# Kernel tuning notes

Measured on AMD Instinct MI355X. Metric: run time of the kernel, lower is better.

## Reference

```python
import jax, jax.numpy as jnp
import numpy as np

DIN = 1024   # input_embedding_size
D = 128      # embedding_size
N, T = 4, 4096


def setup_inputs() -> dict:
    key = jax.random.key(0)
    kx, kq, kk, kv = jax.random.split(key, 4)
    x = jax.random.normal(kx, (N, T, DIN), dtype=jnp.float32)
    # torch Linear(DIN, D, bias=False): weight [D, DIN], y = x @ W.T.
    # Store transposed [DIN, D] so q = x @ Wq is the same math.
    s = 1.0 / np.sqrt(DIN)
    Wq = jax.random.uniform(kq, (DIN, D), jnp.float32, -s, s)
    Wk = jax.random.uniform(kk, (DIN, D), jnp.float32, -s, s)
    Wv = jax.random.uniform(kv, (DIN, D), jnp.float32, -s, s)
    return {"x": x, "Wq": Wq, "Wk": Wk, "Wv": Wv}


def reference(x, Wq, Wk, Wv):
    # x: [N,T,DIN]
    q = jnp.einsum('ntc,cd->ntd', x, Wq)  # [N,T,D]
    k = jnp.einsum('ntc,cd->ntd', x, Wk)
    v = jnp.einsum('ntc,cd->ntd', x, Wv)
    att = jnp.einsum('ntd,nsd->nts', q, k)  # [N,T,T], no 1/sqrt(D) scaling (faithful)
    Tlen = x.shape[1]
    causal = jnp.tril(jnp.ones((Tlen, Tlen), dtype=bool))
    # faithful to torch: tril() zeros upper triangle, then masked_fill(att == 0, -inf)
    att = jnp.where(causal, att, 0.0)
    att = jnp.where(att == 0.0, -jnp.inf, att)
    att = jax.nn.softmax(att, axis=-1)  # [N,T,T]
    out = jnp.einsum('nts,nsd->ntd', att, v)  # [N,T,D]
    return out, att
```

## Files before the change

### kernel.cpp

```cpp
#include <hip/hip_runtime.h>

typedef _Float16 f16;
typedef __attribute__((ext_vector_type(8))) _Float16 f16x8;
typedef __attribute__((ext_vector_type(8))) short s16x8;
typedef __attribute__((ext_vector_type(4))) float f32x4;
typedef __attribute__((ext_vector_type(4))) unsigned short us16x4;

#define DIN   1024
#define DD    128
#define NBAT  4
#define TLEN  4096
#define NROWS (NBAT * TLEN)

static __device__ __forceinline__ unsigned short f2bf(float f) {
  unsigned int u = __builtin_bit_cast(unsigned int, f);
  u = (u + 0x7fffu + ((u >> 16) & 1u)) >> 16;
  return (unsigned short)u;
}
static __device__ __forceinline__ float bf2f(unsigned short h) {
  return __builtin_bit_cast(float, (unsigned int)h << 16);
}
static __device__ __forceinline__ unsigned short f2h(float f) {
  _Float16 h = (_Float16)f;
  return __builtin_bit_cast(unsigned short, h);
}

static __device__ __forceinline__ int swz128(int d, int key) {
  return ((((d >> 3) ^ key) & 15) << 3) | (d & 7);
}
static __device__ __forceinline__ int swz64(int c, int key) {
  return ((((c >> 3) ^ key) & 7) << 3) | (c & 7);
}

typedef __attribute__((address_space(1))) const unsigned int* gas1_t;
typedef __attribute__((address_space(3))) unsigned int* las3_t;
static __device__ __forceinline__ void gload16(const void* g, void* l) {
  __builtin_amdgcn_global_load_lds((gas1_t)g, (las3_t)l, 16, 0, 0);
}

__global__ void build_wt(const float* __restrict__ Wq, const float* __restrict__ Wk,
                         const float* __restrict__ Wv,
                         unsigned short* __restrict__ Wh, unsigned short* __restrict__ Wl) {
  int col = blockIdx.x;
  const float* W = (col < 128) ? Wq : (col < 256 ? Wk : Wv);
  int j = col & 127;
  for (int kk = (int)threadIdx.x; kk < DIN; kk += blockDim.x) {
    float w = W[(size_t)kk * DD + j];
    unsigned short h = f2bf(w);
    unsigned short l = f2bf(w - bf2f(h));
    int c64 = kk >> 6, w64 = kk & 63;
    int kks = (c64 << 6) + swz64(w64, col & 7);
    Wh[(size_t)col * DIN + kks] = h;
    Wl[(size_t)col * DIN + kks] = l;
  }
}

__global__ __launch_bounds__(256, 2) void proj_qkv(
    const float* __restrict__ x,
    const unsigned short* __restrict__ Wh, const unsigned short* __restrict__ Wl,
    unsigned short* __restrict__ qws, unsigned short* __restrict__ kws,
    unsigned short* __restrict__ vws) {
  __shared__ __align__(16) unsigned short Ah[128 * 64];
  __shared__ __align__(16) unsigned short Al[128 * 64];
  __shared__ __align__(16) unsigned short Bh[128 * 64];
  __shared__ __align__(16) unsigned short Bl[128 * 64];

  const int tid = (int)threadIdx.x;
  const int lane = tid & 63;
  const int wid = tid >> 6;
  const int t0 = blockIdx.x * 128;
  const int ct = blockIdx.y;

  const int rbase = (wid >> 1) * 64;
  const int cbase = (wid & 1) * 64;

  f32x4 acc[4][4];
#pragma unroll
  for (int m = 0; m < 4; ++m)
#pragma unroll
    for (int n = 0; n < 4; ++n) acc[m][n] = f32x4{0.f, 0.f, 0.f, 0.f};

  for (int kr = 0; kr < 16; ++kr) {
#pragma unroll
    for (int rr = 0; rr < 8; ++rr) {
      int idx = rr * 256 + tid;
      int row = idx >> 4;
      int c0 = (idx & 15) * 4;
      f32x4 xv = *(const f32x4*)(x + (size_t)(t0 + row) * DIN + kr * 64 + c0);
      int g = swz64(c0, row & 7);
      unsigned short hs0 = f2bf(xv[0]), hs1 = f2bf(xv[1]), hs2 = f2bf(xv[2]), hs3 = f2bf(xv[3]);
      us16x4 hv = {hs0, hs1, hs2, hs3};
      us16x4 lv = {f2bf(xv[0] - bf2f(hs0)), f2bf(xv[1] - bf2f(hs1)),
                   f2bf(xv[2] - bf2f(hs2)), f2bf(xv[3] - bf2f(hs3))};
      *(us16x4*)&Ah[row * 64 + g] = hv;
      *(us16x4*)&Al[row * 64 + g] = lv;
    }
#pragma unroll
    for (int rr = 0; rr < 4; ++rr) {
      int idx = rr * 256 + tid;
      int row = idx >> 3;
      int g = idx & 7;
      size_t gbyte = ((size_t)(ct * 128 + row) * DIN + (size_t)kr * 64) * 2 + (size_t)g * 16;
      gload16((const char*)Wh + gbyte, (char*)Bh + (size_t)idx * 16);
      gload16((const char*)Wl + gbyte, (char*)Bl + (size_t)idx * 16);
    }
    __syncthreads();

#pragma unroll
    for (int kc = 0; kc < 2; ++kc) {
      s16x8 ah[4], al[4], bh[4], bl[4];
#pragma unroll
      for (int m = 0; m < 4; ++m) {
        int r = rbase + m * 16 + (lane & 15);
        int g = ((kc * 4 + (lane >> 4)) ^ (r & 7)) * 8;
        ah[m] = *(const s16x8*)&Ah[r * 64 + g];
        al[m] = *(const s16x8*)&Al[r * 64 + g];
      }
#pragma unroll
      for (int n = 0; n < 4; ++n) {
        int c = cbase + n * 16 + (lane & 15);
        int g = ((kc * 4 + (lane >> 4)) ^ (c & 7)) * 8;
        bh[n] = *(const s16x8*)&Bh[c * 64 + g];
        bl[n] = *(const s16x8*)&Bl[c * 64 + g];
      }
#pragma unroll
      for (int m = 0; m < 4; ++m)
#pragma unroll
        for (int n = 0; n < 4; ++n) {
          acc[m][n] = __builtin_amdgcn_mfma_f32_16x16x32_bf16(ah[m], bh[n], acc[m][n], 0, 0, 0);
          acc[m][n] = __builtin_amdgcn_mfma_f32_16x16x32_bf16(ah[m], bl[n], acc[m][n], 0, 0, 0);
          acc[m][n] = __builtin_amdgcn_mfma_f32_16x16x32_bf16(al[m], bh[n], acc[m][n], 0, 0, 0);
        }
    }
    __syncthreads();
  }

#pragma unroll
  for (int m = 0; m < 4; ++m)
#pragma unroll
    for (int n = 0; n < 4; ++n)
#pragma unroll
      for (int e = 0; e < 4; ++e) {
        int t = t0 + rbase + m * 16 + (lane >> 4) * 4 + e;
        int d = cbase + n * 16 + (lane & 15);
        unsigned short hv = f2h(acc[m][n][e]);
        if (ct == 0) {
          qws[(size_t)t * DD + swz128(d, t & 7)] = hv;
        } else if (ct == 1) {
          kws[(size_t)t * DD + swz128(d, t & 7)] = hv;
        } else {
          int nb = t >> 12, tl = t & (TLEN - 1);
          int ch = tl >> 7, wpos = tl & 127;
          int tls = ch * 128 + swz128(wpos, d & 7);
          vws[((size_t)nb * DD + d) * TLEN + tls] = hv;
        }
      }
}

__global__ __launch_bounds__(256, 2) void attn_fused(
    const unsigned short* __restrict__ qws, const unsigned short* __restrict__ kws,
    const unsigned short* __restrict__ vws, float* __restrict__ out,
    float* __restrict__ att) {
  __shared__ __align__(16) unsigned short kl[128 * 128];
  __shared__ __align__(16) unsigned short vl[128 * 128];
  __shared__ __align__(16) unsigned short qp[64 * 128];

  const int tid = (int)threadIdx.x;
  const int lane = tid & 63;
  const int wid = tid >> 6;
  const int qi = blockIdx.x;
  const int n = blockIdx.y;
  const int t0 = qi * 64;

  {
    const char* gq = (const char*)(qws + (size_t)(n * TLEN + t0) * DD);
#pragma unroll
    for (int rr = 0; rr < 4; ++rr) {
      int idx = rr * 256 + tid;
      gload16(gq + (size_t)idx * 16, (char*)qp + (size_t)idx * 16);
    }
  }
  __syncthreads();
  f16x8 qa[4];
  {
    int r = wid * 16 + (lane & 15);
#pragma unroll
    for (int kc = 0; kc < 4; ++kc) {
      int g = ((kc * 4 + (lane >> 4)) ^ (r & 7)) * 8;
      qa[kc] = *(const f16x8*)&qp[r * 128 + g];
    }
  }
  __syncthreads();

  const int jmax = (t0 + 63) >> 7;
  const int rowg0 = t0 + wid * 16 + (lane >> 4) * 4;

  float zacc[4] = {0.f, 0.f, 0.f, 0.f};
  for (int j = 0; j <= jmax; ++j) {
    const char* gk = (const char*)(kws + (size_t)(n * TLEN + j * 128) * DD);
#pragma unroll
    for (int rr = 0; rr < 8; ++rr) {
      int idx = rr * 256 + tid;
      gload16(gk + (size_t)idx * 16, (char*)kl + (size_t)idx * 16);
    }
    __syncthreads();
#pragma unroll
    for (int fc = 0; fc < 8; ++fc) {
      f32x4 s = f32x4{0.f, 0.f, 0.f, 0.f};
      int rc = fc * 16 + (lane & 15);
#pragma unroll
      for (int kc = 0; kc < 4; ++kc) {
        int g = ((kc * 4 + (lane >> 4)) ^ (rc & 7)) * 8;
        f16x8 kb = *(const f16x8*)&kl[rc * 128 + g];
        s = __builtin_amdgcn_mfma_f32_16x16x32_f16(qa[kc], kb, s, 0, 0, 0);
      }
      int colg = j * 128 + rc;
#pragma unroll
      for (int e = 0; e < 4; ++e) {
        float sv = s[e];
        int rowg = rowg0 + e;
        float ev = (colg <= rowg && sv != 0.0f) ? __expf(sv) : 0.0f;
        zacc[e] += ev;
      }
    }
    __syncthreads();
  }
  float rz[4];
#pragma unroll
  for (int e = 0; e < 4; ++e) {
    float z = zacc[e];
    z += __shfl_xor(z, 1);
    z += __shfl_xor(z, 2);
    z += __shfl_xor(z, 4);
    z += __shfl_xor(z, 8);
    rz[e] = (z > 0.f) ? (1.0f / z) : 0.0f;
  }

  f32x4 oacc[8];
#pragma unroll
  for (int fd = 0; fd < 8; ++fd) oacc[fd] = f32x4{0.f, 0.f, 0.f, 0.f};
  float* attn_base = att + (size_t)n * TLEN * TLEN;

  for (int j = 0; j <= jmax; ++j) {
    const char* gk = (const char*)(kws + (size_t)(n * TLEN + j * 128) * DD);
#pragma unroll
    for (int rr = 0; rr < 8; ++rr) {
      int idx = rr * 256 + tid;
      gload16(gk + (size_t)idx * 16, (char*)kl + (size_t)idx * 16);
    }
    {
      const char* gv = (const char*)(vws + (size_t)n * DD * TLEN);
#pragma unroll
      for (int rr = 0; rr < 8; ++rr) {
        int idx = rr * 256 + tid;
        int d = idx >> 4;
        size_t gb = ((size_t)d * TLEN + (size_t)j * 128) * 2 + (size_t)(idx & 15) * 16;
        gload16(gv + gb, (char*)vl + (size_t)idx * 16);
      }
    }
    __syncthreads();

#pragma unroll
    for (int fc = 0; fc < 8; ++fc) {
      f32x4 s = f32x4{0.f, 0.f, 0.f, 0.f};
      int cloc = fc * 16 + (lane & 15);
#pragma unroll
      for (int kc = 0; kc < 4; ++kc) {
        int g = ((kc * 4 + (lane >> 4)) ^ (cloc & 7)) * 8;
        f16x8 kb = *(const f16x8*)&kl[cloc * 128 + g];
        s = __builtin_amdgcn_mfma_f32_16x16x32_f16(qa[kc], kb, s, 0, 0, 0);
      }
      int colg = j * 128 + cloc;
#pragma unroll
      for (int e = 0; e < 4; ++e) {
        float sv = s[e];
        int rowg = rowg0 + e;
        float ev = (colg <= rowg && sv != 0.0f) ? __expf(sv) : 0.0f;
        float p = ev * rz[e];
        int rq = wid * 16 + (lane >> 4) * 4 + e;
        qp[rq * 128 + swz128(cloc, rq & 7)] = f2h(p);
        attn_base[(size_t)rowg * TLEN + colg] = p;
      }
    }
    __syncthreads();

#pragma unroll
    for (int kc = 0; kc < 4; ++kc) {
      int rp = wid * 16 + (lane & 15);
      int gp = ((kc * 4 + (lane >> 4)) ^ (rp & 7)) * 8;
      f16x8 pa = *(const f16x8*)&qp[rp * 128 + gp];
#pragma unroll
      for (int fd = 0; fd < 8; ++fd) {
        int dv = fd * 16 + (lane & 15);
        int gvv = ((kc * 4 + (lane >> 4)) ^ (dv & 7)) * 8;
        f16x8 vb = *(const f16x8*)&vl[dv * 128 + gvv];
        oacc[fd] = __builtin_amdgcn_mfma_f32_16x16x32_f16(pa, vb, oacc[fd], 0, 0, 0);
      }
    }
    __syncthreads();
  }

#pragma unroll
  for (int fd = 0; fd < 8; ++fd)
#pragma unroll
    for (int e = 0; e < 4; ++e) {
      int t = t0 + wid * 16 + (lane >> 4) * 4 + e;
      int d = fd * 16 + (lane & 15);
      out[(size_t)(n * TLEN + t) * DD + d] = oacc[fd][e];
    }

  int c0 = (jmax + 1) * 128;
  f32x4 z4 = f32x4{0.f, 0.f, 0.f, 0.f};
  for (int r = 0; r < 64; ++r) {
    float* rowp = attn_base + (size_t)(t0 + r) * TLEN;
    for (int c = c0 + tid * 4; c < TLEN; c += 1024) {
      *(f32x4*)(rowp + c) = z4;
    }
  }
}

extern "C" void kernel_launch(void* const* d_in, const int* in_sizes, int n_in,
                              void* d_out, int out_size, void* d_ws, size_t ws_size,
                              hipStream_t stream) {
  const float* x  = (const float*)d_in[0];
  const float* Wq = (const float*)d_in[1];
  const float* Wk = (const float*)d_in[2];
  const float* Wv = (const float*)d_in[3];

  float* out = (float*)d_out;
  float* att = out + (size_t)NBAT * TLEN * DD;

  unsigned short* ws = (unsigned short*)d_ws;
  unsigned short* Wh  = ws;
  unsigned short* Wl  = Wh + (size_t)384 * DIN;
  unsigned short* qws = Wl + (size_t)384 * DIN;
  unsigned short* kws = qws + (size_t)NROWS * DD;
  unsigned short* vws = kws + (size_t)NROWS * DD;

  build_wt<<<dim3(384), dim3(256), 0, stream>>>(Wq, Wk, Wv, Wh, Wl);
  proj_qkv<<<dim3(128, 3), dim3(256), 0, stream>>>(x, Wh, Wl, qws, kws, vws);
  attn_fused<<<dim3(64, 4), dim3(256), 0, stream>>>(qws, kws, vws, out, att);
}
```

Measured before the change: 499.3 us.

## Rewrite projection and attention with small tiles, direct global loads and balanced scheduling

```diff
diff --git a/kernel.cpp b/kernel.cpp
--- a/kernel.cpp
+++ b/kernel.cpp
@@ -4,13 +4,11 @@
 typedef __attribute__((ext_vector_type(8))) _Float16 f16x8;
 typedef __attribute__((ext_vector_type(8))) short s16x8;
 typedef __attribute__((ext_vector_type(4))) float f32x4;
-typedef __attribute__((ext_vector_type(4))) unsigned short us16x4;
 
 #define DIN   1024
 #define DD    128
 #define NBAT  4
 #define TLEN  4096
-#define NROWS (NBAT * TLEN)
 
 static __device__ __forceinline__ unsigned short f2bf(float f) {
   unsigned int u = __builtin_bit_cast(unsigned int, f);
@@ -23,19 +21,6 @@
 static __device__ __forceinline__ unsigned short f2h(float f) {
   _Float16 h = (_Float16)f;
   return __builtin_bit_cast(unsigned short, h);
-}
-
-static __device__ __forceinline__ int swz128(int d, int key) {
-  return ((((d >> 3) ^ key) & 15) << 3) | (d & 7);
-}
-static __device__ __forceinline__ int swz64(int c, int key) {
-  return ((((c >> 3) ^ key) & 7) << 3) | (c & 7);
-}
-
-typedef __attribute__((address_space(1))) const unsigned int* gas1_t;
-typedef __attribute__((address_space(3))) unsigned int* las3_t;
-static __device__ __forceinline__ void gload16(const void* g, void* l) {
-  __builtin_amdgcn_global_load_lds((gas1_t)g, (las3_t)l, 16, 0, 0);
 }
 
 __global__ void build_wt(const float* __restrict__ Wq, const float* __restrict__ Wk,
@@ -48,10 +33,8 @@
     float w = W[(size_t)kk * DD + j];
     unsigned short h = f2bf(w);
     unsigned short l = f2bf(w - bf2f(h));
-    int c64 = kk >> 6, w64 = kk & 63;
-    int kks = (c64 << 6) + swz64(w64, col & 7);
-    Wh[(size_t)col * DIN + kks] = h;
-    Wl[(size_t)col * DIN + kks] = l;
+    Wh[(size_t)col * DIN + kk] = h;
+    Wl[(size_t)col * DIN + kk] = l;
   }
 }
 
@@ -60,172 +43,129 @@
     const unsigned short* __restrict__ Wh, const unsigned short* __restrict__ Wl,
     unsigned short* __restrict__ qws, unsigned short* __restrict__ kws,
     unsigned short* __restrict__ vws) {
-  __shared__ __align__(16) unsigned short Ah[128 * 64];
-  __shared__ __align__(16) unsigned short Al[128 * 64];
-  __shared__ __align__(16) unsigned short Bh[128 * 64];
-  __shared__ __align__(16) unsigned short Bl[128 * 64];
+  __shared__ __align__(16) unsigned short vt[128 * 40];
 
   const int tid = (int)threadIdx.x;
   const int lane = tid & 63;
   const int wid = tid >> 6;
-  const int t0 = blockIdx.x * 128;
-  const int ct = blockIdx.y;
-
-  const int rbase = (wid >> 1) * 64;
-  const int cbase = (wid & 1) * 64;
-
-  f32x4 acc[4][4];
-#pragma unroll
-  for (int m = 0; m < 4; ++m)
-#pragma unroll
-    for (int n = 0; n < 4; ++n) acc[m][n] = f32x4{0.f, 0.f, 0.f, 0.f};
-
-  for (int kr = 0; kr < 16; ++kr) {
-#pragma unroll
-    for (int rr = 0; rr < 8; ++rr) {
-      int idx = rr * 256 + tid;
-      int row = idx >> 4;
-      int c0 = (idx & 15) * 4;
-      f32x4 xv = *(const f32x4*)(x + (size_t)(t0 + row) * DIN + kr * 64 + c0);
-      int g = swz64(c0, row & 7);
-      unsigned short hs0 = f2bf(xv[0]), hs1 = f2bf(xv[1]), hs2 = f2bf(xv[2]), hs3 = f2bf(xv[3]);
-      us16x4 hv = {hs0, hs1, hs2, hs3};
-      us16x4 lv = {f2bf(xv[0] - bf2f(hs0)), f2bf(xv[1] - bf2f(hs1)),
-                   f2bf(xv[2] - bf2f(hs2)), f2bf(xv[3] - bf2f(hs3))};
-      *(us16x4*)&Ah[row * 64 + g] = hv;
-      *(us16x4*)&Al[row * 64 + g] = lv;
-    }
-#pragma unroll
-    for (int rr = 0; rr < 4; ++rr) {
-      int idx = rr * 256 + tid;
-      int row = idx >> 3;
-      int g = idx & 7;
-      size_t gbyte = ((size_t)(ct * 128 + row) * DIN + (size_t)kr * 64) * 2 + (size_t)g * 16;
-      gload16((const char*)Wh + gbyte, (char*)Bh + (size_t)idx * 16);
-      gload16((const char*)Wl + gbyte, (char*)Bl + (size_t)idx * 16);
-    }
-    __syncthreads();
-
-#pragma unroll
-    for (int kc = 0; kc < 2; ++kc) {
-      s16x8 ah[4], al[4], bh[4], bl[4];
-#pragma unroll
-      for (int m = 0; m < 4; ++m) {
-        int r = rbase + m * 16 + (lane & 15);
-        int g = ((kc * 4 + (lane >> 4)) ^ (r & 7)) * 8;
-        ah[m] = *(const s16x8*)&Ah[r * 64 + g];
-        al[m] = *(const s16x8*)&Al[r * 64 + g];
+  const int t0 = blockIdx.x * 32;
+  const int mf = wid >> 1;
+  const int cf0 = (wid & 1) * 12;
+  const int lrow = mf * 16 + (lane & 15);
+  const int ksl = (lane >> 4) * 8;
+
+  f32x4 acc[12];
+#pragma unroll
+  for (int i = 0; i < 12; ++i) acc[i] = f32x4{0.f, 0.f, 0.f, 0.f};
+
+  const float* xrow = x + (size_t)(t0 + lrow) * DIN + ksl;
+
+  for (int kc = 0; kc < 32; ++kc) {
+    f32x4 a0 = *(const f32x4*)(xrow + kc * 32);
+    f32x4 a1 = *(const f32x4*)(xrow + kc * 32 + 4);
+    s16x8 ah, al;
+#pragma unroll
+    for (int e = 0; e < 4; ++e) {
+      unsigned short h0 = f2bf(a0[e]);
+      ah[e] = (short)h0;
+      al[e] = (short)f2bf(a0[e] - bf2f(h0));
+      unsigned short h1 = f2bf(a1[e]);
+      ah[4 + e] = (short)h1;
+      al[4 + e] = (short)f2bf(a1[e] - bf2f(h1));
+    }
+#pragma unroll
+    for (int cf = 0; cf < 12; ++cf) {
+      size_t off = (size_t)((cf0 + cf) * 16 + (lane & 15)) * DIN + (size_t)kc * 32 + ksl;
+      s16x8 bh = *(const s16x8*)(Wh + off);
+      s16x8 bl = *(const s16x8*)(Wl + off);
+      acc[cf] = __builtin_amdgcn_mfma_f32_16x16x32_bf16(ah, bh, acc[cf], 0, 0, 0);
+      acc[cf] = __builtin_amdgcn_mfma_f32_16x16x32_bf16(ah, bl, acc[cf], 0, 0, 0);
+      acc[cf] = __builtin_amdgcn_mfma_f32_16x16x32_bf16(al, bh, acc[cf], 0, 0, 0);
+    }
+  }
+
+  const int n = t0 >> 12, t0l = t0 & (TLEN - 1);
+#pragma unroll
+  for (int cf = 0; cf < 12; ++cf) {
+    int c = (cf0 + cf) * 16 + (lane & 15);
+#pragma unroll
+    for (int e = 0; e < 4; ++e) {
+      int tl = mf * 16 + (lane >> 4) * 4 + e;
+      unsigned short hv = f2h(acc[cf][e]);
+      if (c < 128) {
+        qws[(size_t)(t0 + tl) * DD + c] = hv;
+      } else if (c < 256) {
+        kws[(size_t)(t0 + tl) * DD + (c - 128)] = hv;
+      } else {
+        vt[(c - 256) * 40 + tl] = hv;
       }
-#pragma unroll
-      for (int n = 0; n < 4; ++n) {
-        int c = cbase + n * 16 + (lane & 15);
-        int g = ((kc * 4 + (lane >> 4)) ^ (c & 7)) * 8;
-        bh[n] = *(const s16x8*)&Bh[c * 64 + g];
-        bl[n] = *(const s16x8*)&Bl[c * 64 + g];
-      }
-#pragma unroll
-      for (int m = 0; m < 4; ++m)
-#pragma unroll
-        for (int n = 0; n < 4; ++n) {
-          acc[m][n] = __builtin_amdgcn_mfma_f32_16x16x32_bf16(ah[m], bh[n], acc[m][n], 0, 0, 0);
-          acc[m][n] = __builtin_amdgcn_mfma_f32_16x16x32_bf16(ah[m], bl[n], acc[m][n], 0, 0, 0);
-          acc[m][n] = __builtin_amdgcn_mfma_f32_16x16x32_bf16(al[m], bh[n], acc[m][n], 0, 0, 0);
-        }
-    }
-    __syncthreads();
-  }
-
-#pragma unroll
-  for (int m = 0; m < 4; ++m)
-#pragma unroll
-    for (int n = 0; n < 4; ++n)
-#pragma unroll
-      for (int e = 0; e < 4; ++e) {
-        int t = t0 + rbase + m * 16 + (lane >> 4) * 4 + e;
-        int d = cbase + n * 16 + (lane & 15);
-        unsigned short hv = f2h(acc[m][n][e]);
-        if (ct == 0) {
-          qws[(size_t)t * DD + swz128(d, t & 7)] = hv;
-        } else if (ct == 1) {
-          kws[(size_t)t * DD + swz128(d, t & 7)] = hv;
-        } else {
-          int nb = t >> 12, tl = t & (TLEN - 1);
-          int ch = tl >> 7, wpos = tl & 127;
-          int tls = ch * 128 + swz128(wpos, d & 7);
-          vws[((size_t)nb * DD + d) * TLEN + tls] = hv;
-        }
-      }
-}
-
-__global__ __launch_bounds__(256, 2) void attn_fused(
+    }
+  }
+  __syncthreads();
+  if (tid < 128) {
+    int d = tid;
+    unsigned short* dst = vws + ((size_t)n * DD + d) * TLEN + t0l;
+#pragma unroll
+    for (int h = 0; h < 4; ++h) {
+      f16x8 vv = *(const f16x8*)&vt[d * 40 + h * 8];
+      *(f16x8*)(dst + h * 8) = vv;
+    }
+  }
+}
+
+__global__ __launch_bounds__(256, 4) void attn_fused(
     const unsigned short* __restrict__ qws, const unsigned short* __restrict__ kws,
     const unsigned short* __restrict__ vws, float* __restrict__ out,
     float* __restrict__ att) {
-  __shared__ __align__(16) unsigned short kl[128 * 128];
-  __shared__ __align__(16) unsigned short vl[128 * 128];
-  __shared__ __align__(16) unsigned short qp[64 * 128];
+  __shared__ __align__(16) unsigned short pb[2][16 * 128];
+  __shared__ float zbuf[4][16];
+  __shared__ float rzbuf[16];
 
   const int tid = (int)threadIdx.x;
   const int lane = tid & 63;
   const int wid = tid >> 6;
-  const int qi = blockIdx.x;
-  const int n = blockIdx.y;
-  const int t0 = qi * 64;
-
-  {
-    const char* gq = (const char*)(qws + (size_t)(n * TLEN + t0) * DD);
-#pragma unroll
-    for (int rr = 0; rr < 4; ++rr) {
-      int idx = rr * 256 + tid;
-      gload16(gq + (size_t)idx * 16, (char*)qp + (size_t)idx * 16);
-    }
-  }
-  __syncthreads();
+
+  int b = (int)blockIdx.x;
+  int cr = (b < 512) ? (2 * b) : (2 * (1023 - b) + 1);
+  const int qi = cr >> 2;
+  const int n = cr & 3;
+  const int t0 = qi * 16;
+  const int c0w = wid * 32;
+  const int rl0 = (lane >> 4) * 4;
+  const int ksl = (lane >> 4) * 8;
+
+  const unsigned short* kbase = kws + (size_t)n * TLEN * DD;
+  const unsigned short* vbase = vws + (size_t)n * DD * TLEN;
+
   f16x8 qa[4];
   {
-    int r = wid * 16 + (lane & 15);
-#pragma unroll
-    for (int kc = 0; kc < 4; ++kc) {
-      int g = ((kc * 4 + (lane >> 4)) ^ (r & 7)) * 8;
-      qa[kc] = *(const f16x8*)&qp[r * 128 + g];
-    }
-  }
-  __syncthreads();
-
-  const int jmax = (t0 + 63) >> 7;
-  const int rowg0 = t0 + wid * 16 + (lane >> 4) * 4;
+    const unsigned short* q0 = qws + (size_t)(n * TLEN + t0 + (lane & 15)) * DD + ksl;
+#pragma unroll
+    for (int kc = 0; kc < 4; ++kc) qa[kc] = *(const f16x8*)(q0 + kc * 32);
+  }
+  const int jmax = (t0 + 15) >> 7;
 
   float zacc[4] = {0.f, 0.f, 0.f, 0.f};
   for (int j = 0; j <= jmax; ++j) {
-    const char* gk = (const char*)(kws + (size_t)(n * TLEN + j * 128) * DD);
-#pragma unroll
-    for (int rr = 0; rr < 8; ++rr) {
-      int idx = rr * 256 + tid;
-      gload16(gk + (size_t)idx * 16, (char*)kl + (size_t)idx * 16);
-    }
-    __syncthreads();
-#pragma unroll
-    for (int fc = 0; fc < 8; ++fc) {
-      f32x4 s = f32x4{0.f, 0.f, 0.f, 0.f};
-      int rc = fc * 16 + (lane & 15);
-#pragma unroll
-      for (int kc = 0; kc < 4; ++kc) {
-        int g = ((kc * 4 + (lane >> 4)) ^ (rc & 7)) * 8;
-        f16x8 kb = *(const f16x8*)&kl[rc * 128 + g];
-        s = __builtin_amdgcn_mfma_f32_16x16x32_f16(qa[kc], kb, s, 0, 0, 0);
-      }
-      int colg = j * 128 + rc;
-#pragma unroll
-      for (int e = 0; e < 4; ++e) {
-        float sv = s[e];
-        int rowg = rowg0 + e;
-        float ev = (colg <= rowg && sv != 0.0f) ? __expf(sv) : 0.0f;
-        zacc[e] += ev;
-      }
-    }
-    __syncthreads();
-  }
-  float rz[4];
+    f32x4 s0 = f32x4{0.f, 0.f, 0.f, 0.f};
+    f32x4 s1 = f32x4{0.f, 0.f, 0.f, 0.f};
+    const unsigned short* kt = kbase + (size_t)(j * 128 + c0w + (lane & 15)) * DD + ksl;
+#pragma unroll
+    for (int kc = 0; kc < 4; ++kc) {
+      f16x8 kb0 = *(const f16x8*)(kt + kc * 32);
+      f16x8 kb1 = *(const f16x8*)(kt + 16 * DD + kc * 32);
+      s0 = __builtin_amdgcn_mfma_f32_16x16x32_f16(qa[kc], kb0, s0, 0, 0, 0);
+      s1 = __builtin_amdgcn_mfma_f32_16x16x32_f16(qa[kc], kb1, s1, 0, 0, 0);
+    }
+    int colg0 = j * 128 + c0w + (lane & 15);
+#pragma unroll
+    for (int e = 0; e < 4; ++e) {
+      int rowg = t0 + rl0 + e;
+      float ev0 = (colg0 <= rowg && s0[e] != 0.0f) ? __expf(s0[e]) : 0.0f;
+      float ev1 = (colg0 + 16 <= rowg && s1[e] != 0.0f) ? __expf(s1[e]) : 0.0f;
+      zacc[e] += ev0 + ev1;
+    }
+  }
 #pragma unroll
   for (int e = 0; e < 4; ++e) {
     float z = zacc[e];
@@ -233,88 +173,90 @@
     z += __shfl_xor(z, 2);
     z += __shfl_xor(z, 4);
     z += __shfl_xor(z, 8);
-    rz[e] = (z > 0.f) ? (1.0f / z) : 0.0f;
-  }
-
-  f32x4 oacc[8];
-#pragma unroll
-  for (int fd = 0; fd < 8; ++fd) oacc[fd] = f32x4{0.f, 0.f, 0.f, 0.f};
-  float* attn_base = att + (size_t)n * TLEN * TLEN;
+    if ((lane & 15) == 0) zbuf[wid][rl0 + e] = z;
+  }
+  __syncthreads();
+  if (tid < 16) {
+    float z = zbuf[0][tid] + zbuf[1][tid] + zbuf[2][tid] + zbuf[3][tid];
+    rzbuf[tid] = (z > 0.f) ? (1.0f / z) : 0.0f;
+  }
+  __syncthreads();
+  float rz[4];
+#pragma unroll
+  for (int e = 0; e < 4; ++e) rz[e] = rzbuf[rl0 + e];
+
+  f32x4 oacc0 = f32x4{0.f, 0.f, 0.f, 0.f};
+  f32x4 oacc1 = f32x4{0.f, 0.f, 0.f, 0.f};
+  float* attn_base = att + (size_t)n * TLEN * TLEN + (size_t)t0 * TLEN;
+  int cur = 0;
 
   for (int j = 0; j <= jmax; ++j) {
-    const char* gk = (const char*)(kws + (size_t)(n * TLEN + j * 128) * DD);
-#pragma unroll
-    for (int rr = 0; rr < 8; ++rr) {
-      int idx = rr * 256 + tid;
-      gload16(gk + (size_t)idx * 16, (char*)kl + (size_t)idx * 16);
-    }
+    f32x4 s0 = f32x4{0.f, 0.f, 0.f, 0.f};
+    f32x4 s1 = f32x4{0.f, 0.f, 0.f, 0.f};
+    const unsigned short* kt = kbase + (size_t)(j * 128 + c0w + (lane & 15)) * DD + ksl;
+#pragma unroll
+    for (int kc = 0; kc < 4; ++kc) {
+      f16x8 kb0 = *(const f16x8*)(kt + kc * 32);
+      f16x8 kb1 = *(const f16x8*)(kt + 16 * DD + kc * 32);
+      s0 = __builtin_amdgcn_mfma_f32_16x16x32_f16(qa[kc], kb0, s0, 0, 0, 0);
+      s1 = __builtin_amdgcn_mfma_f32_16x16x32_f16(qa[kc], kb1, s1, 0, 0, 0);
+    }
+    unsigned short* pw = pb[cur];
+    int colg0 = j * 128 + c0w + (lane & 15);
+#pragma unroll
+    for (int e = 0; e < 4; ++e) {
+      int rowg = t0 + rl0 + e;
+      int rl = rl0 + e;
+      float ev0 = (colg0 <= rowg && s0[e] != 0.0f) ? __expf(s0[e]) : 0.0f;
+      float ev1 = (colg0 + 16 <= rowg && s1[e] != 0.0f) ? __expf(s1[e]) : 0.0f;
+      int c0 = c0w + (lane & 15);
+      int c1 = c0 + 16;
+      pw[rl * 128 + ((((c0 >> 3) ^ (rl & 7)) << 3) | (c0 & 7))] = f2h(ev0 * rz[e]);
+      pw[rl * 128 + ((((c1 >> 3) ^ (rl & 7)) << 3) | (c1 & 7))] = f2h(ev1 * rz[e]);
+    }
+    __syncthreads();
+
     {
-      const char* gv = (const char*)(vws + (size_t)n * DD * TLEN);
-#pragma unroll
-      for (int rr = 0; rr < 8; ++rr) {
-        int idx = rr * 256 + tid;
-        int d = idx >> 4;
-        size_t gb = ((size_t)d * TLEN + (size_t)j * 128) * 2 + (size_t)(idx & 15) * 16;
-        gload16(gv + gb, (char*)vl + (size_t)idx * 16);
+      int r = tid >> 4, c8 = tid & 15;
+      f16x8 pv = *(const f16x8*)&pw[r * 128 + (((c8 ^ (r & 7)) & 15) << 3)];
+      f32x4 o0, o1;
+#pragma unroll
+      for (int i = 0; i < 4; ++i) {
+        o0[i] = (float)pv[i];
+        o1[i] = (float)pv[4 + i];
       }
-    }
-    __syncthreads();
-
-#pragma unroll
-    for (int fc = 0; fc < 8; ++fc) {
-      f32x4 s = f32x4{0.f, 0.f, 0.f, 0.f};
-      int cloc = fc * 16 + (lane & 15);
-#pragma unroll
-      for (int kc = 0; kc < 4; ++kc) {
-        int g = ((kc * 4 + (lane >> 4)) ^ (cloc & 7)) * 8;
-        f16x8 kb = *(const f16x8*)&kl[cloc * 128 + g];
-        s = __builtin_amdgcn_mfma_f32_16x16x32_f16(qa[kc], kb, s, 0, 0, 0);
-      }
-      int colg = j * 128 + cloc;
-#pragma unroll
-      for (int e = 0; e < 4; ++e) {
-        float sv = s[e];
-        int rowg = rowg0 + e;
-        float ev = (colg <= rowg && sv != 0.0f) ? __expf(sv) : 0.0f;
-        float p = ev * rz[e];
-        int rq = wid * 16 + (lane >> 4) * 4 + e;
-        qp[rq * 128 + swz128(cloc, rq & 7)] = f2h(p);
-        attn_base[(size_t)rowg * TLEN + colg] = p;
-      }
-    }
-    __syncthreads();
+      float* dst = attn_base + (size_t)r * TLEN + j * 128 + c8 * 8;
+      *(f32x4*)dst = o0;
+      *(f32x4*)(dst + 4) = o1;
+    }
 
 #pragma unroll
     for (int kc = 0; kc < 4; ++kc) {
-      int rp = wid * 16 + (lane & 15);
-      int gp = ((kc * 4 + (lane >> 4)) ^ (rp & 7)) * 8;
-      f16x8 pa = *(const f16x8*)&qp[rp * 128 + gp];
-#pragma unroll
-      for (int fd = 0; fd < 8; ++fd) {
-        int dv = fd * 16 + (lane & 15);
-        int gvv = ((kc * 4 + (lane >> 4)) ^ (dv & 7)) * 8;
-        f16x8 vb = *(const f16x8*)&vl[dv * 128 + gvv];
-        oacc[fd] = __builtin_amdgcn_mfma_f32_16x16x32_f16(pa, vb, oacc[fd], 0, 0, 0);
-      }
-    }
-    __syncthreads();
-  }
-
-#pragma unroll
-  for (int fd = 0; fd < 8; ++fd)
-#pragma unroll
-    for (int e = 0; e < 4; ++e) {
-      int t = t0 + wid * 16 + (lane >> 4) * 4 + e;
-      int d = fd * 16 + (lane & 15);
-      out[(size_t)(n * TLEN + t) * DD + d] = oacc[fd][e];
-    }
-
-  int c0 = (jmax + 1) * 128;
-  f32x4 z4 = f32x4{0.f, 0.f, 0.f, 0.f};
-  for (int r = 0; r < 64; ++r) {
-    float* rowp = attn_base + (size_t)(t0 + r) * TLEN;
-    for (int c = c0 + tid * 4; c < TLEN; c += 1024) {
-      *(f32x4*)(rowp + c) = z4;
+      int rp = lane & 15;
+      f16x8 pa = *(const f16x8*)&pw[rp * 128 + ((((kc * 4 + (lane >> 4)) ^ (rp & 7)) & 15) << 3)];
+      const unsigned short* vt0 = vbase + (size_t)(c0w + (lane & 15)) * TLEN + (size_t)j * 128 + kc * 32 + ksl;
+      f16x8 vb0 = *(const f16x8*)(vt0);
+      f16x8 vb1 = *(const f16x8*)(vt0 + (size_t)16 * TLEN);
+      oacc0 = __builtin_amdgcn_mfma_f32_16x16x32_f16(pa, vb0, oacc0, 0, 0, 0);
+      oacc1 = __builtin_amdgcn_mfma_f32_16x16x32_f16(pa, vb1, oacc1, 0, 0, 0);
+    }
+    cur ^= 1;
+  }
+
+#pragma unroll
+  for (int e = 0; e < 4; ++e) {
+    int t = t0 + rl0 + e;
+    float* orow = out + ((size_t)n * TLEN + t) * DD;
+    orow[c0w + (lane & 15)] = oacc0[e];
+    orow[c0w + 16 + (lane & 15)] = oacc1[e];
+  }
+
+  int cz0 = (jmax + 1) * 128;
+  f32x4 zv = f32x4{0.f, 0.f, 0.f, 0.f};
+  for (int r = 0; r < 16; ++r) {
+    float* rowp = attn_base + (size_t)r * TLEN;
+    for (int c = cz0 + tid * 4; c < TLEN; c += 1024) {
+      *(f32x4*)(rowp + c) = zv;
     }
   }
 }
@@ -334,10 +276,10 @@
   unsigned short* Wh  = ws;
   unsigned short* Wl  = Wh + (size_t)384 * DIN;
   unsigned short* qws = Wl + (size_t)384 * DIN;
-  unsigned short* kws = qws + (size_t)NROWS * DD;
-  unsigned short* vws = kws + (size_t)NROWS * DD;
+  unsigned short* kws = qws + (size_t)NBAT * TLEN * DD;
+  unsigned short* vws = kws + (size_t)NBAT * TLEN * DD;
 
   build_wt<<<dim3(384), dim3(256), 0, stream>>>(Wq, Wk, Wv, Wh, Wl);
-  proj_qkv<<<dim3(128, 3), dim3(256), 0, stream>>>(x, Wh, Wl, qws, kws, vws);
-  attn_fused<<<dim3(64, 4), dim3(256), 0, stream>>>(qws, kws, vws, out, att);
-}
+  proj_qkv<<<dim3(512), dim3(256), 0, stream>>>(x, Wh, Wl, qws, kws, vws);
+  attn_fused<<<dim3(1024), dim3(256), 0, stream>>>(qws, kws, vws, out, att);
+}
```

After: 669.5 us. 34.1% more time.
